# Kernel tuning notes

Hardware: AMD Instinct MI355X
Metric: run time of the kernel (lower is better)

Reference implementation:

```python
import jax, jax.numpy as jnp
import numpy as np

BS, R, W, N, H = 256, 4, 128, 2048, 256
TAU, ALPHA, EPS = 1.0, 0.7, 1e-8


def _l2norm(x, axis):
    return x / (jnp.linalg.norm(x, axis=axis, keepdims=True) + EPS)


def _gumbel(u):
    # standard Gumbel(0,1) from uniform samples
    return -jnp.log(-jnp.log(u + 1e-10) + 1e-10)


def setup_inputs() -> dict:
    key = jax.random.key(0)
    ks = jax.random.split(key, 10)
    return {
        "k_r": jax.random.normal(ks[0], (BS, R * W), jnp.float32),
        "m_t": jax.random.normal(ks[1], (BS, W), jnp.float32),
        "hx": jax.random.normal(ks[2], (1, BS, H), jnp.float32),
        "memory": jax.random.uniform(ks[3], (BS, W, N), jnp.float32),
        "usage": jax.random.uniform(ks[4], (BS, N), jnp.float32),
        "read_weights": jax.random.uniform(ks[5], (BS, R, N), jnp.float32),
        "Wg": jax.random.normal(ks[6], (H, 1), jnp.float32) / np.float32(np.sqrt(H)),
        "bg": jnp.zeros((1,), jnp.float32),
        "noise_write": jax.random.uniform(ks[7], (BS, 1, N), jnp.float32),
        "noise_read": jax.random.uniform(ks[8], (BS, R, N), jnp.float32),
        "m_idx": jax.random.randint(ks[9], (BS, N), 0, N).astype(jnp.int64),
        "seq_idx": N,
    }


def reference(k_r, m_t, hx, memory, usage, read_weights, Wg, bg,
              noise_write, noise_read, m_idx, seq_idx):
    # --- key / candidate preprocessing ---
    read_keys = jnp.tanh(k_r.reshape(BS, R, W))   # bs r W
    write_m = jnp.tanh(m_t.reshape(BS, 1, W))     # bs 1 W

    # --- usage bookkeeping (read weights detached as in torch) ---
    u_t = ALPHA * usage + (1.0 - ALPHA) * jax.lax.stop_gradient(read_weights).sum(axis=1)  # bs N

    # --- write (memory-full branch: content-addressed erase/update) ---
    # reversed cosine similarity between candidate and each slot
    dist = jnp.einsum('biw,bwn->bin', _l2norm(write_m, 2), _l2norm(memory, 1))  # bs 1 N
    gamma = jax.nn.sigmoid(hx[-1] @ Wg + bg)                                    # bs 1
    soft_wt = -dist + (gamma * u_t)[:, None, :]                                 # bs 1 N
    write_wt = jax.nn.softmax((1.0 - soft_wt + _gumbel(noise_write)) / TAU, axis=2)  # bs 1 N

    m_erased = jnp.einsum('bin,bwn->biw', write_wt, memory)                     # bs 1 W
    # M * (E - e^T w) + m^T w  with e = ones -> M*(1 - w) + m^T w
    mem_new = memory * (1.0 - write_wt) + jnp.einsum('biw,bin->bwn', write_m, write_wt)
    usage_new = u_t * (1.0 - jax.lax.stop_gradient(write_wt[:, 0, :]))          # bs N

    # --- read (gumbel-softmax content addressing on updated memory) ---
    dist_r = jnp.einsum('brw,bwn->brn', _l2norm(read_keys, 2), _l2norm(mem_new, 1))  # bs r N
    read_wt = jax.nn.softmax((dist_r + _gumbel(noise_read)) / TAU, axis=2)           # bs r N
    m_read = jnp.einsum('brn,bwn->brw', read_wt, mem_new)                            # bs r W

    return (m_read, mem_new, usage_new, read_wt, m_erased)
```

## Files before the change

kernel.cpp:

```cpp
#include <hip/hip_runtime.h>

#define BS   256
#define RR   4
#define WW   128
#define NN   2048
#define HH   256
#define NT   512
#define WH   64
#define NWAVE (NT / 64)

__device__ __forceinline__ float wave_sum(float v) {
#pragma unroll
  for (int m = 32; m >= 1; m >>= 1) v += __shfl_xor(v, m, 64);
  return v;
}
__device__ __forceinline__ float wave_max(float v) {
#pragma unroll
  for (int m = 32; m >= 1; m >>= 1) v = fmaxf(v, __shfl_xor(v, m, 64));
  return v;
}
__device__ __forceinline__ float block_sum(float v, float* s_red) {
  const int tid = threadIdx.x;
  v = wave_sum(v);
  __syncthreads();
  if ((tid & 63) == 0) s_red[tid >> 6] = v;
  __syncthreads();
  float s = s_red[0];
#pragma unroll
  for (int i = 1; i < NWAVE; ++i) s += s_red[i];
  return s;
}
__device__ __forceinline__ float block_max(float v, float* s_red) {
  const int tid = threadIdx.x;
  v = wave_max(v);
  __syncthreads();
  if ((tid & 63) == 0) s_red[tid >> 6] = v;
  __syncthreads();
  float s = s_red[0];
#pragma unroll
  for (int i = 1; i < NWAVE; ++i) s = fmaxf(s, s_red[i]);
  return s;
}
__device__ __forceinline__ void block_max4(float v[RR], float* s_red4) {
  const int tid = threadIdx.x, lane = tid & 63, wid = tid >> 6;
#pragma unroll
  for (int m = 32; m >= 1; m >>= 1) {
#pragma unroll
    for (int r = 0; r < RR; ++r) v[r] = fmaxf(v[r], __shfl_xor(v[r], m, 64));
  }
  __syncthreads();
  if (lane == 0) {
#pragma unroll
    for (int r = 0; r < RR; ++r) s_red4[wid * RR + r] = v[r];
  }
  __syncthreads();
#pragma unroll
  for (int r = 0; r < RR; ++r) {
    float s = s_red4[r];
#pragma unroll
    for (int i = 1; i < NWAVE; ++i) s = fmaxf(s, s_red4[i * RR + r]);
    v[r] = s;
  }
}
__device__ __forceinline__ void block_sum4(float v[RR], float* s_red4) {
  const int tid = threadIdx.x, lane = tid & 63, wid = tid >> 6;
#pragma unroll
  for (int m = 32; m >= 1; m >>= 1) {
#pragma unroll
    for (int r = 0; r < RR; ++r) v[r] += __shfl_xor(v[r], m, 64);
  }
  __syncthreads();
  if (lane == 0) {
#pragma unroll
    for (int r = 0; r < RR; ++r) s_red4[wid * RR + r] = v[r];
  }
  __syncthreads();
#pragma unroll
  for (int r = 0; r < RR; ++r) {
    float s = s_red4[r];
#pragma unroll
    for (int i = 1; i < NWAVE; ++i) s += s_red4[i * RR + r];
    v[r] = s;
  }
}
__device__ __forceinline__ float gumbelf(float u) {
  return -logf(-logf(u + 1e-10f) + 1e-10f);
}

#define STAT(base, rh, comp, b) ((base) + ((size_t)((rh)*6 + (comp)) * BS + (b)) * NN)

__global__ __launch_bounds__(NT, 4) void k1_stats(
    const float* __restrict__ k_r, const float* __restrict__ m_t,
    const float* __restrict__ memory, float* __restrict__ stats)
{
  __shared__ float s_wm[WH];
  __shared__ float s_rk[RR][WH];
  const int bid = blockIdx.x;
  const int b = bid >> 1, rh = bid & 1;
  const int tid = threadIdx.x;
  const int c0 = 4 * tid;

  if (tid < WH) {
    s_wm[tid] = tanhf(m_t[(size_t)b * WW + rh * WH + tid]);
  } else if (tid < WH + RR * WH) {
    const int i = tid - WH;
    s_rk[i >> 6][i & 63] =
        tanhf(k_r[(size_t)b * RR * WW + (i >> 6) * WW + rh * WH + (i & 63)]);
  }
  __syncthreads();

  const float* Mb = memory + (size_t)b * WW * NN + (size_t)rh * WH * NN;
  float cn[4] = {0.f, 0.f, 0.f, 0.f}, wd[4] = {0.f, 0.f, 0.f, 0.f};
  float rdM[RR][4];
#pragma unroll
  for (int r = 0; r < RR; ++r) {
#pragma unroll
    for (int j = 0; j < 4; ++j) rdM[r][j] = 0.f;
  }
#pragma unroll 8
  for (int w = 0; w < WH; ++w) {
    float4 v = *reinterpret_cast<const float4*>(Mb + (size_t)w * NN + c0);
    const float wmw = s_wm[w];
    cn[0] = fmaf(v.x, v.x, cn[0]); wd[0] = fmaf(wmw, v.x, wd[0]);
    cn[1] = fmaf(v.y, v.y, cn[1]); wd[1] = fmaf(wmw, v.y, wd[1]);
    cn[2] = fmaf(v.z, v.z, cn[2]); wd[2] = fmaf(wmw, v.z, wd[2]);
    cn[3] = fmaf(v.w, v.w, cn[3]); wd[3] = fmaf(wmw, v.w, wd[3]);
#pragma unroll
    for (int r = 0; r < RR; ++r) {
      const float rkw = s_rk[r][w];
      rdM[r][0] = fmaf(rkw, v.x, rdM[r][0]);
      rdM[r][1] = fmaf(rkw, v.y, rdM[r][1]);
      rdM[r][2] = fmaf(rkw, v.z, rdM[r][2]);
      rdM[r][3] = fmaf(rkw, v.w, rdM[r][3]);
    }
  }
  float4 o;
  o.x = cn[0]; o.y = cn[1]; o.z = cn[2]; o.w = cn[3];
  *reinterpret_cast<float4*>(STAT(stats, rh, 0, b) + c0) = o;
  o.x = wd[0]; o.y = wd[1]; o.z = wd[2]; o.w = wd[3];
  *reinterpret_cast<float4*>(STAT(stats, rh, 1, b) + c0) = o;
#pragma unroll
  for (int r = 0; r < RR; ++r) {
    o.x = rdM[r][0]; o.y = rdM[r][1]; o.z = rdM[r][2]; o.w = rdM[r][3];
    *reinterpret_cast<float4*>(STAT(stats, rh, 2 + r, b) + c0) = o;
  }
}

__global__ __launch_bounds__(NT) void k2_softmax(
    const float* __restrict__ k_r, const float* __restrict__ m_t,
    const float* __restrict__ hx, const float* __restrict__ usage,
    const float* __restrict__ read_weights, const float* __restrict__ Wg,
    const float* __restrict__ bg, const float* __restrict__ noise_write,
    const float* __restrict__ noise_read, const float* __restrict__ stats,
    float* __restrict__ wt_out, float* __restrict__ usage_new,
    float* __restrict__ read_wt_out)
{
  __shared__ float s_wm[WW];
  __shared__ float s_rk[RR * WW];
  __shared__ float s_red[NWAVE * RR];
  __shared__ float s_rkinv[RR], s_rkwm[RR];

  const int b = blockIdx.x;
  const int tid = threadIdx.x;
  const int lane = tid & 63;
  const int wid = tid >> 6;
  const int c0 = 4 * tid;

  float gp = 0.f;
  if (tid < HH) gp = hx[(size_t)b * HH + tid] * Wg[tid];
  if (tid < WW) s_wm[tid] = tanhf(m_t[(size_t)b * WW + tid]);
  s_rk[tid] = tanhf(k_r[(size_t)b * (RR * WW) + tid]);

  float ut[4];
  {
    const size_t rb = (size_t)b * RR * NN;
    float4 u4 = *reinterpret_cast<const float4*>(usage + (size_t)b * NN + c0);
    float4 r0 = *reinterpret_cast<const float4*>(read_weights + rb + c0);
    float4 r1 = *reinterpret_cast<const float4*>(read_weights + rb + NN + c0);
    float4 r2 = *reinterpret_cast<const float4*>(read_weights + rb + 2 * NN + c0);
    float4 r3 = *reinterpret_cast<const float4*>(read_weights + rb + 3 * NN + c0);
    ut[0] = 0.7f * u4.x + 0.3f * (r0.x + r1.x + r2.x + r3.x);
    ut[1] = 0.7f * u4.y + 0.3f * (r0.y + r1.y + r2.y + r3.y);
    ut[2] = 0.7f * u4.z + 0.3f * (r0.z + r1.z + r2.z + r3.z);
    ut[3] = 0.7f * u4.w + 0.3f * (r0.w + r1.w + r2.w + r3.w);
  }

  const float gamma = 1.f / (1.f + expf(-(block_sum(gp, s_red) + bg[0])));
  float wmp = (tid < WW) ? s_wm[tid] * s_wm[tid] : 0.f;
  const float wmss = block_sum(wmp, s_red);
  const float inv_wm = 1.f / (sqrtf(wmss) + 1e-8f);

  if (wid < RR) {
    const float a = s_rk[wid * WW + lane];
    const float c = s_rk[wid * WW + 64 + lane];
    const float wa = s_wm[lane], wc = s_wm[64 + lane];
    float ss = wave_sum(a * a + c * c);
    float sw = wave_sum(a * wa + c * wc);
    if (lane == 0) {
      s_rkinv[wid] = 1.f / (sqrtf(ss) + 1e-8f);
      s_rkwm[wid] = sw;
    }
  }
  __syncthreads();

  float cn[4], wd[4], rdM[RR][4];
  {
    float4 a0 = *reinterpret_cast<const float4*>(STAT(stats, 0, 0, b) + c0);
    float4 a1 = *reinterpret_cast<const float4*>(STAT(stats, 1, 0, b) + c0);
    cn[0] = a0.x + a1.x; cn[1] = a0.y + a1.y; cn[2] = a0.z + a1.z; cn[3] = a0.w + a1.w;
    float4 b0 = *reinterpret_cast<const float4*>(STAT(stats, 0, 1, b) + c0);
    float4 b1 = *reinterpret_cast<const float4*>(STAT(stats, 1, 1, b) + c0);
    wd[0] = b0.x + b1.x; wd[1] = b0.y + b1.y; wd[2] = b0.z + b1.z; wd[3] = b0.w + b1.w;
#pragma unroll
    for (int r = 0; r < RR; ++r) {
      float4 d0 = *reinterpret_cast<const float4*>(STAT(stats, 0, 2 + r, b) + c0);
      float4 d1 = *reinterpret_cast<const float4*>(STAT(stats, 1, 2 + r, b) + c0);
      rdM[r][0] = d0.x + d1.x; rdM[r][1] = d0.y + d1.y;
      rdM[r][2] = d0.z + d1.z; rdM[r][3] = d0.w + d1.w;
    }
  }

  float lg[4], mx = -1e30f;
  {
    float4 nw = *reinterpret_cast<const float4*>(noise_write + (size_t)b * NN + c0);
    const float nwv[4] = {nw.x, nw.y, nw.z, nw.w};
#pragma unroll
    for (int j = 0; j < 4; ++j) {
      float dist = wd[j] * inv_wm / (sqrtf(cn[j]) + 1e-8f);
      lg[j] = 1.f + dist - gamma * ut[j] + gumbelf(nwv[j]);
      mx = fmaxf(mx, lg[j]);
    }
  }
  mx = block_max(mx, s_red);
  float ex[4], es = 0.f;
#pragma unroll
  for (int j = 0; j < 4; ++j) { ex[j] = expf(lg[j] - mx); es += ex[j]; }
  es = block_sum(es, s_red);
  const float inv_es = 1.f / es;
  float wtk[4], omw[4];
#pragma unroll
  for (int j = 0; j < 4; ++j) { wtk[j] = ex[j] * inv_es; omw[j] = 1.f - wtk[j]; }
  {
    float4 un, wo;
    un.x = ut[0] * omw[0]; un.y = ut[1] * omw[1];
    un.z = ut[2] * omw[2]; un.w = ut[3] * omw[3];
    *reinterpret_cast<float4*>(usage_new + (size_t)b * NN + c0) = un;
    wo.x = wtk[0]; wo.y = wtk[1]; wo.z = wtk[2]; wo.w = wtk[3];
    *reinterpret_cast<float4*>(wt_out + (size_t)b * NN + c0) = wo;
  }

  const float invrk[RR] = { s_rkinv[0], s_rkinv[1], s_rkinv[2], s_rkinv[3] };
  const float rkwm[RR]  = { s_rkwm[0], s_rkwm[1], s_rkwm[2], s_rkwm[3] };
  float inv_cn2[4];
#pragma unroll
  for (int j = 0; j < 4; ++j) {
    float cn2 = omw[j] * omw[j] * cn[j]
              + 2.f * omw[j] * wtk[j] * wd[j]
              + wtk[j] * wtk[j] * wmss;
    inv_cn2[j] = 1.f / (sqrtf(cn2) + 1e-8f);
  }
  float lr[RR][4], mr[RR];
#pragma unroll
  for (int r = 0; r < RR; ++r) {
    float4 nr = *reinterpret_cast<const float4*>(
        noise_read + ((size_t)b * RR + r) * NN + c0);
    const float nrv[4] = {nr.x, nr.y, nr.z, nr.w};
    float m = -1e30f;
#pragma unroll
    for (int j = 0; j < 4; ++j) {
      float rd = omw[j] * rdM[r][j] + wtk[j] * rkwm[r];
      lr[r][j] = rd * invrk[r] * inv_cn2[j] + gumbelf(nrv[j]);
      m = fmaxf(m, lr[r][j]);
    }
    mr[r] = m;
  }
  block_max4(mr, s_red);
  float er[RR][4], ers[RR];
#pragma unroll
  for (int r = 0; r < RR; ++r) {
    float s = 0.f;
#pragma unroll
    for (int j = 0; j < 4; ++j) { er[r][j] = expf(lr[r][j] - mr[r]); s += er[r][j]; }
    ers[r] = s;
  }
  block_sum4(ers, s_red);
#pragma unroll
  for (int r = 0; r < RR; ++r) {
    const float inv_ers = 1.f / ers[r];
    float4 o;
    o.x = er[r][0] * inv_ers; o.y = er[r][1] * inv_ers;
    o.z = er[r][2] * inv_ers; o.w = er[r][3] * inv_ers;
    *reinterpret_cast<float4*>(read_wt_out + ((size_t)b * RR + r) * NN + c0) = o;
  }
}

__global__ __launch_bounds__(NT, 4) void k3_apply(
    const float* __restrict__ m_t, const float* __restrict__ memory,
    const float* __restrict__ wt_in, const float* __restrict__ read_wt,
    float* __restrict__ mem_new, float* __restrict__ m_read,
    float* __restrict__ m_erased)
{
  __shared__ float s_wm[WH];
  __shared__ float s_mr[WH * RR * NWAVE];
  __shared__ float s_me[WH * NWAVE];

  const int bid = blockIdx.x;
  const int b = bid >> 1, rh = bid & 1;
  const int tid = threadIdx.x;
  const int lane = tid & 63;
  const int wid = tid >> 6;
  const int c0 = 4 * tid;

  if (tid < WH) s_wm[tid] = tanhf(m_t[(size_t)b * WW + rh * WH + tid]);

  float wt[4], omw[4];
  {
    float4 w4 = *reinterpret_cast<const float4*>(wt_in + (size_t)b * NN + c0);
    wt[0] = w4.x; wt[1] = w4.y; wt[2] = w4.z; wt[3] = w4.w;
#pragma unroll
    for (int j = 0; j < 4; ++j) omw[j] = 1.f - wt[j];
  }
  float rwt[RR][4];
#pragma unroll
  for (int r = 0; r < RR; ++r) {
    float4 t = *reinterpret_cast<const float4*>(
        read_wt + ((size_t)b * RR + r) * NN + c0);
    rwt[r][0] = t.x; rwt[r][1] = t.y; rwt[r][2] = t.z; rwt[r][3] = t.w;
  }
  __syncthreads();

  const size_t hbase = (size_t)b * WW * NN + (size_t)rh * WH * NN;
  const float* Mb = memory + hbase;
  float* MNb = mem_new + hbase;

#pragma unroll 2
  for (int w0 = 0; w0 < WH; w0 += 4) {
    float pme[4], mrp[4][RR];
#pragma unroll
    for (int i = 0; i < 4; ++i) {
      const int w = w0 + i;
      const float wmw = s_wm[w];
      const size_t off = (size_t)w * NN + c0;
      float4 v = *reinterpret_cast<const float4*>(Mb + off);
      float4 nv;
      nv.x = fmaf(v.x, omw[0], wmw * wt[0]);
      nv.y = fmaf(v.y, omw[1], wmw * wt[1]);
      nv.z = fmaf(v.z, omw[2], wmw * wt[2]);
      nv.w = fmaf(v.w, omw[3], wmw * wt[3]);
      *reinterpret_cast<float4*>(MNb + off) = nv;
      float p = wt[0] * v.x;
      p = fmaf(wt[1], v.y, p);
      p = fmaf(wt[2], v.z, p);
      p = fmaf(wt[3], v.w, p);
      pme[i] = p;
#pragma unroll
      for (int r = 0; r < RR; ++r) {
        float a = rwt[r][0] * nv.x;
        a = fmaf(rwt[r][1], nv.y, a);
        a = fmaf(rwt[r][2], nv.z, a);
        a = fmaf(rwt[r][3], nv.w, a);
        mrp[i][r] = a;
      }
    }
#pragma unroll
    for (int m = 32; m >= 1; m >>= 1) {
#pragma unroll
      for (int i = 0; i < 4; ++i) {
        pme[i] += __shfl_xor(pme[i], m, 64);
#pragma unroll
        for (int r = 0; r < RR; ++r) mrp[i][r] += __shfl_xor(mrp[i][r], m, 64);
      }
    }
    if (lane == 0) {
#pragma unroll
      for (int i = 0; i < 4; ++i) {
        s_me[(w0 + i) * NWAVE + wid] = pme[i];
#pragma unroll
        for (int r = 0; r < RR; ++r)
          s_mr[((w0 + i) * RR + r) * NWAVE + wid] = mrp[i][r];
      }
    }
  }
  __syncthreads();

  if (tid < WH * RR) {
    const int wl = tid >> 2, r = tid & 3;
    float s = 0.f;
#pragma unroll
    for (int i = 0; i < NWAVE; ++i) s += s_mr[(wl * RR + r) * NWAVE + i];
    m_read[(size_t)b * RR * WW + r * WW + rh * WH + wl] = s;
  } else if (tid < WH * RR + WH) {
    const int wl = tid - WH * RR;
    float s = 0.f;
#pragma unroll
    for (int i = 0; i < NWAVE; ++i) s += s_me[wl * NWAVE + i];
    m_erased[(size_t)b * WW + rh * WH + wl] = s;
  }
}

extern "C" void kernel_launch(void* const* d_in, const int* in_sizes, int n_in,
                              void* d_out, int out_size, void* d_ws, size_t ws_size,
                              hipStream_t stream) {
  (void)in_sizes; (void)n_in; (void)ws_size; (void)out_size;
  const float* k_r          = (const float*)d_in[0];
  const float* m_t          = (const float*)d_in[1];
  const float* hx           = (const float*)d_in[2];
  const float* memory       = (const float*)d_in[3];
  const float* usage        = (const float*)d_in[4];
  const float* read_weights = (const float*)d_in[5];
  const float* Wg           = (const float*)d_in[6];
  const float* bg           = (const float*)d_in[7];
  const float* noise_write  = (const float*)d_in[8];
  const float* noise_read   = (const float*)d_in[9];

  float* out       = (float*)d_out;
  float* m_read    = out;
  float* mem_new   = m_read + (size_t)BS * RR * WW;
  float* usage_new = mem_new + (size_t)BS * WW * NN;
  float* read_wt   = usage_new + (size_t)BS * NN;
  float* m_erased  = read_wt + (size_t)BS * RR * NN;

  float* stats = mem_new;
  float* wt_ws = (float*)d_ws;

  k1_stats<<<dim3(2 * BS), dim3(NT), 0, stream>>>(k_r, m_t, memory, stats);
  k2_softmax<<<dim3(BS), dim3(NT), 0, stream>>>(
      k_r, m_t, hx, usage, read_weights, Wg, bg, noise_write, noise_read,
      stats, wt_ws, usage_new, read_wt);
  k3_apply<<<dim3(2 * BS), dim3(NT), 0, stream>>>(
      m_t, memory, wt_ws, read_wt, mem_new, m_read, m_erased);
}
```

Baseline: 186.6 us.

## Restructure k3_apply so each wave owns memory rows and accumulates across columns

Each wave now takes a fixed group of 8 memory rows and walks all 2048 columns, keeping running partial sums in registers. The cross-lane shuffle reduction therefore happens once per row instead of once per row group, and the cross-wave shared-memory reduction goes away. Write and read weights are staged in shared memory, and mem_new is written with nontemporal stores. The cost is more registers per thread, since launch bounds drop to 2 blocks per SM, and therefore less occupancy to hide the latency of the streaming memory loads.

Result: faster. 170.3 us (-8.7%).

```diff
diff --git a/kernel.cpp b/kernel.cpp
--- a/kernel.cpp
+++ b/kernel.cpp
@@ -8,6 +8,9 @@
 #define NT   512
 #define WH   64
 #define NWAVE (NT / 64)
+#define RPW  (WH / NWAVE)
+
+typedef float nfloat4 __attribute__((ext_vector_type(4)));
 
 __device__ __forceinline__ float wave_sum(float v) {
 #pragma unroll
@@ -294,107 +297,109 @@
   }
 }
 
-__global__ __launch_bounds__(NT, 4) void k3_apply(
+__global__ __launch_bounds__(NT, 2) void k3_apply(
     const float* __restrict__ m_t, const float* __restrict__ memory,
     const float* __restrict__ wt_in, const float* __restrict__ read_wt,
     float* __restrict__ mem_new, float* __restrict__ m_read,
     float* __restrict__ m_erased)
 {
-  __shared__ float s_wm[WH];
-  __shared__ float s_mr[WH * RR * NWAVE];
-  __shared__ float s_me[WH * NWAVE];
+  __shared__ float s_wt[NN];
+  __shared__ float s_rwt[RR][NN];
 
   const int bid = blockIdx.x;
   const int b = bid >> 1, rh = bid & 1;
   const int tid = threadIdx.x;
   const int lane = tid & 63;
   const int wid = tid >> 6;
-  const int c0 = 4 * tid;
-
-  if (tid < WH) s_wm[tid] = tanhf(m_t[(size_t)b * WW + rh * WH + tid]);
-
-  float wt[4], omw[4];
+
   {
-    float4 w4 = *reinterpret_cast<const float4*>(wt_in + (size_t)b * NN + c0);
-    wt[0] = w4.x; wt[1] = w4.y; wt[2] = w4.z; wt[3] = w4.w;
-#pragma unroll
-    for (int j = 0; j < 4; ++j) omw[j] = 1.f - wt[j];
-  }
-  float rwt[RR][4];
-#pragma unroll
-  for (int r = 0; r < RR; ++r) {
-    float4 t = *reinterpret_cast<const float4*>(
-        read_wt + ((size_t)b * RR + r) * NN + c0);
-    rwt[r][0] = t.x; rwt[r][1] = t.y; rwt[r][2] = t.z; rwt[r][3] = t.w;
-  }
+    const int c = 4 * tid;
+    float4 w4 = *reinterpret_cast<const float4*>(wt_in + (size_t)b * NN + c);
+    *reinterpret_cast<float4*>(&s_wt[c]) = w4;
+#pragma unroll
+    for (int r = 0; r < RR; ++r) {
+      float4 t = *reinterpret_cast<const float4*>(
+          read_wt + ((size_t)b * RR + r) * NN + c);
+      *reinterpret_cast<float4*>(&s_rwt[r][c]) = t;
+    }
+  }
+  const int w0 = wid * RPW;
+  float wm[RPW];
+#pragma unroll
+  for (int i = 0; i < RPW; ++i)
+    wm[i] = tanhf(m_t[(size_t)b * WW + rh * WH + w0 + i]);
   __syncthreads();
 
   const size_t hbase = (size_t)b * WW * NN + (size_t)rh * WH * NN;
   const float* Mb = memory + hbase;
   float* MNb = mem_new + hbase;
 
-#pragma unroll 2
-  for (int w0 = 0; w0 < WH; w0 += 4) {
-    float pme[4], mrp[4][RR];
-#pragma unroll
-    for (int i = 0; i < 4; ++i) {
-      const int w = w0 + i;
-      const float wmw = s_wm[w];
-      const size_t off = (size_t)w * NN + c0;
+  float pme[RPW];
+  float mrp[RPW][RR];
+#pragma unroll
+  for (int i = 0; i < RPW; ++i) {
+    pme[i] = 0.f;
+#pragma unroll
+    for (int r = 0; r < RR; ++r) mrp[i][r] = 0.f;
+  }
+
+#pragma unroll 1
+  for (int ch = 0; ch < NN; ch += 256) {
+    const int c = ch + 4 * lane;
+    const float4 wt4 = *reinterpret_cast<const float4*>(&s_wt[c]);
+    const float ow0 = 1.f - wt4.x, ow1 = 1.f - wt4.y,
+                ow2 = 1.f - wt4.z, ow3 = 1.f - wt4.w;
+    float4 rw[RR];
+#pragma unroll
+    for (int r = 0; r < RR; ++r)
+      rw[r] = *reinterpret_cast<const float4*>(&s_rwt[r][c]);
+
+#pragma unroll
+    for (int i = 0; i < RPW; ++i) {
+      const size_t off = (size_t)(w0 + i) * NN + c;
       float4 v = *reinterpret_cast<const float4*>(Mb + off);
       float4 nv;
-      nv.x = fmaf(v.x, omw[0], wmw * wt[0]);
-      nv.y = fmaf(v.y, omw[1], wmw * wt[1]);
-      nv.z = fmaf(v.z, omw[2], wmw * wt[2]);
-      nv.w = fmaf(v.w, omw[3], wmw * wt[3]);
-      *reinterpret_cast<float4*>(MNb + off) = nv;
-      float p = wt[0] * v.x;
-      p = fmaf(wt[1], v.y, p);
-      p = fmaf(wt[2], v.z, p);
-      p = fmaf(wt[3], v.w, p);
-      pme[i] = p;
+      nv.x = fmaf(v.x, ow0, wm[i] * wt4.x);
+      nv.y = fmaf(v.y, ow1, wm[i] * wt4.y);
+      nv.z = fmaf(v.z, ow2, wm[i] * wt4.z);
+      nv.w = fmaf(v.w, ow3, wm[i] * wt4.w);
+      nfloat4 nvv;
+      nvv.x = nv.x; nvv.y = nv.y; nvv.z = nv.z; nvv.w = nv.w;
+      __builtin_nontemporal_store(nvv, reinterpret_cast<nfloat4*>(MNb + off));
+      float p = wt4.x * v.x;
+      p = fmaf(wt4.y, v.y, p);
+      p = fmaf(wt4.z, v.z, p);
+      p = fmaf(wt4.w, v.w, p);
+      pme[i] += p;
 #pragma unroll
       for (int r = 0; r < RR; ++r) {
-        float a = rwt[r][0] * nv.x;
-        a = fmaf(rwt[r][1], nv.y, a);
-        a = fmaf(rwt[r][2], nv.z, a);
-        a = fmaf(rwt[r][3], nv.w, a);
-        mrp[i][r] = a;
+        float a = rw[r].x * nv.x;
+        a = fmaf(rw[r].y, nv.y, a);
+        a = fmaf(rw[r].z, nv.z, a);
+        a = fmaf(rw[r].w, nv.w, a);
+        mrp[i][r] += a;
       }
     }
-#pragma unroll
-    for (int m = 32; m >= 1; m >>= 1) {
-#pragma unroll
-      for (int i = 0; i < 4; ++i) {
-        pme[i] += __shfl_xor(pme[i], m, 64);
-#pragma unroll
-        for (int r = 0; r < RR; ++r) mrp[i][r] += __shfl_xor(mrp[i][r], m, 64);
-      }
-    }
-    if (lane == 0) {
-#pragma unroll
-      for (int i = 0; i < 4; ++i) {
-        s_me[(w0 + i) * NWAVE + wid] = pme[i];
-#pragma unroll
-        for (int r = 0; r < RR; ++r)
-          s_mr[((w0 + i) * RR + r) * NWAVE + wid] = mrp[i][r];
-      }
-    }
-  }
-  __syncthreads();
-
-  if (tid < WH * RR) {
-    const int wl = tid >> 2, r = tid & 3;
-    float s = 0.f;
-#pragma unroll
-    for (int i = 0; i < NWAVE; ++i) s += s_mr[(wl * RR + r) * NWAVE + i];
-    m_read[(size_t)b * RR * WW + r * WW + rh * WH + wl] = s;
-  } else if (tid < WH * RR + WH) {
-    const int wl = tid - WH * RR;
-    float s = 0.f;
-#pragma unroll
-    for (int i = 0; i < NWAVE; ++i) s += s_me[wl * NWAVE + i];
-    m_erased[(size_t)b * WW + rh * WH + wl] = s;
+  }
+
+#pragma unroll
+  for (int m = 32; m >= 1; m >>= 1) {
+#pragma unroll
+    for (int i = 0; i < RPW; ++i) {
+      pme[i] += __shfl_xor(pme[i], m, 64);
+#pragma unroll
+      for (int r = 0; r < RR; ++r) mrp[i][r] += __shfl_xor(mrp[i][r], m, 64);
+    }
+  }
+  if (lane == 0) {
+    const int wg = rh * WH + w0;
+#pragma unroll
+    for (int i = 0; i < RPW; ++i) {
+      m_erased[(size_t)b * WW + wg + i] = pme[i];
+#pragma unroll
+      for (int r = 0; r < RR; ++r)
+        m_read[(size_t)b * RR * WW + r * WW + wg + i] = mrp[i][r];
+    }
   }
 }
 
```
